# Performance work log

Measured on AMD Instinct MI355X. Metric: run time of the kernel, lower is better.

Reference implementation:

```python
import jax, jax.numpy as jnp
import numpy as np

WS = 2
D = 128  # hidden_dim per direction
SCALE_X = float(np.sqrt(2.0))  # rescale=True, highway_bias=0 -> sqrt(1+exp(0))


def sru_bidir(x, W, wc, b, k):
    """Bidirectional single-layer SRU (sru lib, layer_norm=False, rescale=True).
    x: (L, N, din). Returns (L, N, 2*D)."""
    L, N, _ = x.shape
    U = (x @ W).reshape(L, N, 2, D, k)  # (L,N,dir,D,k)
    vf, vr = wc.reshape(2, 2, D)  # each (dir, D)
    bf, br = b.reshape(2, 2, D)
    # time-reverse the backward direction so one scan handles both
    U = jnp.concatenate([U[:, :, :1], U[::-1, :, 1:]], axis=2)
    if k == 4:
        xprime = U[..., 3]
    else:
        xp = x.reshape(L, N, 2, D)
        xprime = jnp.concatenate([xp[:, :, :1], xp[::-1, :, 1:]], axis=2) * SCALE_X

    def step(c, inp):
        u0, u1, u2, xpt = inp  # each (N,2,D)
        f = jax.nn.sigmoid(u1 + vf * c + bf)
        c = f * c + (1.0 - f) * u0
        r = jax.nn.sigmoid(u2 + vr * c + br)
        h = r * c + (1.0 - r) * xpt
        return c, h

    c0 = jnp.zeros((N, 2, D), dtype=x.dtype)
    _, H = jax.lax.scan(step, c0, (U[..., 0], U[..., 1], U[..., 2], xprime))
    # un-reverse backward direction outputs
    H = jnp.concatenate([H[:, :, :1], H[::-1, :, 1:]], axis=2)
    return H.reshape(L, N, 2 * D)


def setup_inputs() -> dict:
    key = jax.random.key(0)
    ks = jax.random.split(key, 6)
    B, C, Himg, Wimg = 8, 3, 224, 224
    F = WS * WS * C  # 12
    inp = {
        "x": jax.random.normal(ks[0], (B, C, Himg, Wimg), jnp.float32),
        "W1": jax.random.normal(ks[1], (F, 2 * D * 4), jnp.float32) * (1.0 / np.sqrt(F)),
        "wc1": jax.random.normal(ks[2], (2 * 2 * D,), jnp.float32) * 0.1,
        "b1": jnp.zeros((2 * 2 * D,), jnp.float32),
        "W2": jax.random.normal(ks[3], (2 * D, 2 * D * 3), jnp.float32) * (1.0 / np.sqrt(2 * D)),
        "wc2": jax.random.normal(ks[4], (2 * 2 * D,), jnp.float32) * 0.1,
        "b2": jnp.zeros((2 * 2 * D,), jnp.float32),
    }
    return inp


def reference(x, W1, wc1, b1, W2, wc2, b2):
    B, C, Himg, Wimg = x.shape
    Hp, Wp = Himg // WS, Wimg // WS
    F = WS * WS * C
    # get_valid_patches: (B, Hp, Wp, C*ws*ws) with (C, wh, ww) flatten order
    p = x.reshape(B, C, Hp, WS, Wp, WS).transpose(0, 2, 4, 1, 3, 5).reshape(B, Hp, Wp, F)
    # input_array = patches.permute(2,0,3,1) -> (Hp, B, Wp, F)
    # apply_one_direction on firstVRNN: merge Hp into batch, scan over Wp
    a1 = p.transpose(1, 0, 2, 3).reshape(Hp * B, Wp, F).transpose(1, 0, 2)  # (Wp, Hp*B, F)
    h1 = sru_bidir(a1, W1, wc1, b1, k=4)  # (Wp, Hp*B, 2D)
    h1 = h1.transpose(1, 0, 2).reshape(Hp, B, Wp, 2 * D)
    # vertical_results = out.permute(2,1,0,3) -> (Wp, B, Hp, 2D)
    v = h1.transpose(2, 1, 0, 3)
    # second direction: merge Wp into batch, scan over Hp
    a2 = v.reshape(Wp * B, Hp, 2 * D).transpose(1, 0, 2)  # (Hp, Wp*B, 2D)
    h2 = sru_bidir(a2, W2, wc2, b2, k=3)  # (Hp, Wp*B, 2D)
    h2 = h2.transpose(1, 0, 2).reshape(Wp, B, Hp, 2 * D)
    # feature_map.permute(1,3,2,0) -> (B, 2D, Hp, Wp)
    return h2.transpose(1, 3, 2, 0)
```

## Files before the change

### kernel.cpp

```cpp
#include <hip/hip_runtime.h>
#include <hip/hip_bf16.h>

typedef unsigned short ushort_t;
typedef unsigned int uint_t;

typedef __bf16 bf16x8 __attribute__((ext_vector_type(8)));
typedef float f32x4 __attribute__((ext_vector_type(4)));
typedef ushort_t us8 __attribute__((ext_vector_type(8)));

__device__ __forceinline__ float bf2f(ushort_t u) {
    return __uint_as_float(((uint_t)u) << 16);
}
__device__ __forceinline__ ushort_t f2bf(float f) {
    uint_t x = __float_as_uint(f);
    uint_t r = (x + 0x7FFFu + ((x >> 16) & 1u)) >> 16;
    return (ushort_t)r;
}
__device__ __forceinline__ float sigmoidf_fast(float x) {
    return 1.0f / (1.0f + __expf(-x));
}

#define PP 12544
#define PLANE 25690112ULL

__global__ __launch_bounds__(256) void permute_w2(const float* __restrict__ W2,
                                                  ushort_t* __restrict__ W2t) {
    int i = blockIdx.x * 256 + threadIdx.x;
    int np = i >> 8;
    int k  = i & 255;
    int kk  = np >> 8;
    int rem = np & 255;
    int dir = rem >> 7;
    int d   = rem & 127;
    int oc = dir * 384 + d * 3 + kk;
    W2t[np * 256 + k] = f2bf(W2[k * 768 + oc]);
}

__global__ __launch_bounds__(256) void scan1(const float* __restrict__ x,
                                             const float* __restrict__ W1,
                                             const float* __restrict__ wc1,
                                             const float* __restrict__ b1,
                                             ushort_t* __restrict__ H1a) {
    __shared__ float patch[112 * 12];
    const int n1 = blockIdx.x;
    const int hp = n1 >> 3, b = n1 & 7;
    const int tid = threadIdx.x;

    for (int e = tid; e < 1344; e += 256) {
        int c = e / 448;
        int rem = e % 448;
        int wh = rem / 224;
        int pos = rem % 224;
        float v = x[((b * 3 + c) * 224 + (2 * hp + wh)) * 224 + pos];
        patch[(pos >> 1) * 12 + c * 4 + wh * 2 + (pos & 1)] = v;
    }

    float4 w[12];
    const float4* W1v = (const float4*)W1;
#pragma unroll
    for (int j = 0; j < 12; ++j) w[j] = W1v[j * 256 + tid];

    const float vf = wc1[tid],       vr = wc1[256 + tid];
    const float bfv = b1[tid],       brv = b1[256 + tid];
    const int dir = tid >> 7;

    __syncthreads();

    const size_t h1base = ((size_t)b * PP + (size_t)hp * 112) * 256 + tid;

    float cst = 0.0f;
    for (int t = 0; t < 112; ++t) {
        const int tt = dir ? (111 - t) : t;
        const float4* pp = (const float4*)(patch + tt * 12);
        float4 p0 = pp[0], p1 = pp[1], p2 = pp[2];
        float pj[12] = {p0.x, p0.y, p0.z, p0.w, p1.x, p1.y, p1.z, p1.w,
                        p2.x, p2.y, p2.z, p2.w};
        float u0 = 0.f, u1 = 0.f, u2 = 0.f, u3 = 0.f;
#pragma unroll
        for (int j = 0; j < 12; ++j) {
            float pv = pj[j];
            u0 = fmaf(w[j].x, pv, u0);
            u1 = fmaf(w[j].y, pv, u1);
            u2 = fmaf(w[j].z, pv, u2);
            u3 = fmaf(w[j].w, pv, u3);
        }
        float f = sigmoidf_fast(u1 + vf * cst + bfv);
        cst = f * cst + (1.0f - f) * u0;
        float r = sigmoidf_fast(u2 + vr * cst + brv);
        float h = r * cst + (1.0f - r) * u3;
        H1a[h1base + (size_t)tt * 256] = f2bf(h);
    }
}

__global__ __launch_bounds__(256) void gemm2(const ushort_t* __restrict__ A,
                                             const ushort_t* __restrict__ Bt,
                                             ushort_t* __restrict__ U2t) {
    __shared__ ushort_t As[2][128 * 32];
    __shared__ ushort_t Bs[2][128 * 32];

    const int l    = blockIdx.x;
    const int pair = (l & 7) * 588 + (l >> 3);
    const int nx   = pair % 6;
    const int ny   = pair / 6;

    const int m0 = ny * 128;
    const int bb = ny / 98;
    const int p0 = (ny % 98) * 128;
    const int n0 = nx * 128;
    const int kidx = n0 >> 8;
    const int ch0  = n0 & 255;
    const int tid = threadIdx.x;
    const int w = tid >> 6, lane = tid & 63;
    const int wm = w >> 1, wn = w & 1;
    const int lr = lane >> 2;
    const int lc = (lane & 3) * 8;
    const int ln16 = lane & 15;
    const int k8 = (lane >> 4) * 8;

    f32x4 acc[4][4] = {};

    for (int kb = 0; kb < 256; kb += 64) {
        if (kb) __syncthreads();
#pragma unroll
        for (int h = 0; h < 2; ++h) {
#pragma unroll
            for (int q = 0; q < 2; ++q) {
                int r = w * 32 + q * 16;
                const ushort_t* gA = A + (size_t)(m0 + r + lr) * 256 + kb + h * 32 + lc;
                __builtin_amdgcn_global_load_lds(
                    (const __attribute__((address_space(1))) uint_t*)gA,
                    (__attribute__((address_space(3))) uint_t*)(As[h] + r * 32), 16, 0, 0);
                const ushort_t* gB = Bt + (size_t)(n0 + r + lr) * 256 + kb + h * 32 + lc;
                __builtin_amdgcn_global_load_lds(
                    (const __attribute__((address_space(1))) uint_t*)gB,
                    (__attribute__((address_space(3))) uint_t*)(Bs[h] + r * 32), 16, 0, 0);
            }
        }
        __syncthreads();

#pragma unroll
        for (int h = 0; h < 2; ++h) {
            bf16x8 af[4], bf[4];
#pragma unroll
            for (int i = 0; i < 4; ++i) {
                af[i] = *(const bf16x8*)(As[h] + (wm * 64 + i * 16 + ln16) * 32 + k8);
                bf[i] = *(const bf16x8*)(Bs[h] + (wn * 64 + i * 16 + ln16) * 32 + k8);
            }
#pragma unroll
            for (int i = 0; i < 4; ++i)
#pragma unroll
                for (int j = 0; j < 4; ++j)
                    acc[i][j] = __builtin_amdgcn_mfma_f32_16x16x32_bf16(
                        af[i], bf[j], acc[i][j], 0, 0, 0);
        }

        if (nx < 4 && kb == nx * 64) {
            const int cl = tid & 63;
            const int pc = tid >> 6;
            const int hh = cl >> 5;
            const int cc = cl & 31;
            const size_t p3 = 3 * PLANE
                            + (size_t)(bb * 256 + kb + cl) * PP + p0 + pc * 32;
#pragma unroll
            for (int j8 = 0; j8 < 4; ++j8) {
                us8 v;
#pragma unroll
                for (int j = 0; j < 8; ++j)
                    v[j] = As[hh][(pc * 32 + j8 * 8 + j) * 32 + cc];
                *(us8*)(U2t + p3 + j8 * 8) = v;
            }
        }
    }

    const int rq = (lane >> 4) * 4;
    const size_t planeBase = (size_t)kidx * PLANE + (size_t)(bb * 256 + ch0) * PP;
#pragma unroll
    for (int i = 0; i < 4; ++i) {
        int p = p0 + wm * 64 + i * 16 + rq;
#pragma unroll
        for (int j = 0; j < 4; ++j) {
            int ch_l = wn * 64 + j * 16 + ln16;
            ushort4 v;
            v.x = f2bf(acc[i][j][0]);
            v.y = f2bf(acc[i][j][1]);
            v.z = f2bf(acc[i][j][2]);
            v.w = f2bf(acc[i][j][3]);
            *(ushort4*)(U2t + planeBase + (size_t)ch_l * PP + p) = v;
        }
    }
}

__global__ __launch_bounds__(256) void scan2(const ushort_t* __restrict__ U2t,
                                             const float* __restrict__ wc2,
                                             const float* __restrict__ b2,
                                             float* __restrict__ out) {
    const int cb = blockIdx.x;
    const int b  = blockIdx.y;
    const int tid = threadIdx.x;
    const int ch = cb * 2 + (tid >> 7);
    const int wp = tid & 127;
    if (wp >= 112) return;
    const int dir = ch >> 7;
    const float SCALE_X = 1.41421356237309515f;

    const float vf = wc2[ch],  vr = wc2[256 + ch];
    const float bfv = b2[ch],  brv = b2[256 + ch];

    const int tt0 = dir ? 111 : 0;
    const long dstep = dir ? -112 : 112;
    const long ostep = dir ? -112 : 112;

    const ushort_t* P = U2t;
    long oOff = (long)((size_t)(b * 256 + ch) * 112 + tt0) * 112 + wp;

    ushort_t buf[7][4];
    long qp = (long)((size_t)(b * 256 + ch) * PP) + tt0 * 112 + wp;
#pragma unroll
    for (int i = 0; i < 6; ++i) {
        buf[i][0] = P[qp];
        buf[i][1] = P[PLANE + qp];
        buf[i][2] = P[2 * PLANE + qp];
        buf[i][3] = P[3 * PLANE + qp];
        qp += dstep;
    }

    float cst = 0.0f;
    for (int tb = 0; tb < 16; ++tb) {
#pragma unroll
        for (int u = 0; u < 7; ++u) {
            const int t = tb * 7 + u;
            buf[(u + 6) % 7][0] = P[qp];
            buf[(u + 6) % 7][1] = P[PLANE + qp];
            buf[(u + 6) % 7][2] = P[2 * PLANE + qp];
            buf[(u + 6) % 7][3] = P[3 * PLANE + qp];
            qp += (t < 105) ? dstep : 0;

            float u0 = bf2f(buf[u][0]);
            float u1 = bf2f(buf[u][1]);
            float u2v = bf2f(buf[u][2]);
            float xp = bf2f(buf[u][3]) * SCALE_X;
            float f = sigmoidf_fast(u1 + vf * cst + bfv);
            cst = f * cst + (1.0f - f) * u0;
            float r = sigmoidf_fast(u2v + vr * cst + brv);
            out[oOff] = r * cst + (1.0f - r) * xp;
            oOff += ostep;
        }
    }
}

extern "C" void kernel_launch(void* const* d_in, const int* in_sizes, int n_in,
                              void* d_out, int out_size, void* d_ws, size_t ws_size,
                              hipStream_t stream) {
    const float* x   = (const float*)d_in[0];
    const float* W1  = (const float*)d_in[1];
    const float* wc1 = (const float*)d_in[2];
    const float* b1  = (const float*)d_in[3];
    const float* W2  = (const float*)d_in[4];
    const float* wc2 = (const float*)d_in[5];
    const float* b2  = (const float*)d_in[6];
    float* out = (float*)d_out;

    char* ws = (char*)d_ws;
    ushort_t* H1a = (ushort_t*)(ws);
    ushort_t* U2t = (ushort_t*)(ws + 51380224);
    ushort_t* W2t = (ushort_t*)(ws + 51380224 + 205520896);

    permute_w2<<<768, 256, 0, stream>>>(W2, W2t);
    scan1<<<896, 256, 0, stream>>>(x, W1, wc1, b1, H1a);
    gemm2<<<4704, 256, 0, stream>>>(H1a, W2t, U2t);
    scan2<<<dim3(128, 8), 256, 0, stream>>>(U2t, wc2, b2, out);
}
```

Measured before the change: 353.2 us.

## Double-buffer GEMM K-loop with 32-wide stages to overlap loads and MFMA

Restructures the second-layer GEMM main loop from four 64-wide K blocks, each fully loaded before compute, into eight 32-wide stages with ping-pong LDS buffers. The next stage's global-to-LDS loads are issued before the current stage's MFMAs, so memory latency can hide behind compute. Global pointers are hoisted out of the loop, and the x-prime copy-out is adapted to 32-column stages. The cost is more barriers per tile and shallower compute per stage.

```diff
diff --git a/kernel.cpp b/kernel.cpp
--- a/kernel.cpp
+++ b/kernel.cpp
@@ -117,60 +117,76 @@
     const int ln16 = lane & 15;
     const int k8 = (lane >> 4) * 8;
 
+    const int r0 = w * 32;
+    const ushort_t* gA0 = A  + (size_t)(m0 + r0 + lr) * 256 + lc;
+    const ushort_t* gA1 = A  + (size_t)(m0 + r0 + 16 + lr) * 256 + lc;
+    const ushort_t* gB0 = Bt + (size_t)(n0 + r0 + lr) * 256 + lc;
+    const ushort_t* gB1 = Bt + (size_t)(n0 + r0 + 16 + lr) * 256 + lc;
+
     f32x4 acc[4][4] = {};
 
-    for (int kb = 0; kb < 256; kb += 64) {
-        if (kb) __syncthreads();
-#pragma unroll
-        for (int h = 0; h < 2; ++h) {
-#pragma unroll
-            for (int q = 0; q < 2; ++q) {
-                int r = w * 32 + q * 16;
-                const ushort_t* gA = A + (size_t)(m0 + r + lr) * 256 + kb + h * 32 + lc;
-                __builtin_amdgcn_global_load_lds(
-                    (const __attribute__((address_space(1))) uint_t*)gA,
-                    (__attribute__((address_space(3))) uint_t*)(As[h] + r * 32), 16, 0, 0);
-                const ushort_t* gB = Bt + (size_t)(n0 + r + lr) * 256 + kb + h * 32 + lc;
-                __builtin_amdgcn_global_load_lds(
-                    (const __attribute__((address_space(1))) uint_t*)gB,
-                    (__attribute__((address_space(3))) uint_t*)(Bs[h] + r * 32), 16, 0, 0);
-            }
-        }
-        __syncthreads();
-
-#pragma unroll
-        for (int h = 0; h < 2; ++h) {
-            bf16x8 af[4], bf[4];
-#pragma unroll
-            for (int i = 0; i < 4; ++i) {
-                af[i] = *(const bf16x8*)(As[h] + (wm * 64 + i * 16 + ln16) * 32 + k8);
-                bf[i] = *(const bf16x8*)(Bs[h] + (wn * 64 + i * 16 + ln16) * 32 + k8);
-            }
-#pragma unroll
-            for (int i = 0; i < 4; ++i)
-#pragma unroll
-                for (int j = 0; j < 4; ++j)
-                    acc[i][j] = __builtin_amdgcn_mfma_f32_16x16x32_bf16(
-                        af[i], bf[j], acc[i][j], 0, 0, 0);
-        }
-
-        if (nx < 4 && kb == nx * 64) {
-            const int cl = tid & 63;
-            const int pc = tid >> 6;
-            const int hh = cl >> 5;
-            const int cc = cl & 31;
+#define STAGE(bufi, s32)                                                      \
+    do {                                                                      \
+        const int kc_ = (s32) * 32;                                           \
+        __builtin_amdgcn_global_load_lds(                                     \
+            (const __attribute__((address_space(1))) uint_t*)(gA0 + kc_),     \
+            (__attribute__((address_space(3))) uint_t*)(As[bufi] + r0 * 32),  \
+            16, 0, 0);                                                        \
+        __builtin_amdgcn_global_load_lds(                                     \
+            (const __attribute__((address_space(1))) uint_t*)(gA1 + kc_),     \
+            (__attribute__((address_space(3))) uint_t*)(As[bufi] + (r0 + 16) * 32), \
+            16, 0, 0);                                                        \
+        __builtin_amdgcn_global_load_lds(                                     \
+            (const __attribute__((address_space(1))) uint_t*)(gB0 + kc_),     \
+            (__attribute__((address_space(3))) uint_t*)(Bs[bufi] + r0 * 32),  \
+            16, 0, 0);                                                        \
+        __builtin_amdgcn_global_load_lds(                                     \
+            (const __attribute__((address_space(1))) uint_t*)(gB1 + kc_),     \
+            (__attribute__((address_space(3))) uint_t*)(Bs[bufi] + (r0 + 16) * 32), \
+            16, 0, 0);                                                        \
+    } while (0)
+
+    STAGE(0, 0);
+    asm volatile("s_waitcnt vmcnt(0)" ::: "memory");
+    __builtin_amdgcn_s_barrier();
+
+    for (int s = 0; s < 8; ++s) {
+        const int cur = s & 1;
+        if (s < 7) STAGE(cur ^ 1, s + 1);
+
+        bf16x8 af[4], bfr[4];
+#pragma unroll
+        for (int i = 0; i < 4; ++i) {
+            af[i]  = *(const bf16x8*)(As[cur] + (wm * 64 + i * 16 + ln16) * 32 + k8);
+            bfr[i] = *(const bf16x8*)(Bs[cur] + (wn * 64 + i * 16 + ln16) * 32 + k8);
+        }
+#pragma unroll
+        for (int i = 0; i < 4; ++i)
+#pragma unroll
+            for (int j = 0; j < 4; ++j)
+                acc[i][j] = __builtin_amdgcn_mfma_f32_16x16x32_bf16(
+                    af[i], bfr[j], acc[i][j], 0, 0, 0);
+
+        if (nx < 4 && (s >> 1) == nx) {
+            const int cl = tid & 31;
+            const int pc = tid >> 5;
             const size_t p3 = 3 * PLANE
-                            + (size_t)(bb * 256 + kb + cl) * PP + p0 + pc * 32;
-#pragma unroll
-            for (int j8 = 0; j8 < 4; ++j8) {
+                            + (size_t)(bb * 256 + s * 32 + cl) * PP
+                            + p0 + pc * 16;
+#pragma unroll
+            for (int j8 = 0; j8 < 2; ++j8) {
                 us8 v;
 #pragma unroll
                 for (int j = 0; j < 8; ++j)
-                    v[j] = As[hh][(pc * 32 + j8 * 8 + j) * 32 + cc];
+                    v[j] = As[cur][(pc * 16 + j8 * 8 + j) * 32 + cl];
                 *(us8*)(U2t + p3 + j8 * 8) = v;
             }
         }
-    }
+
+        asm volatile("s_waitcnt vmcnt(0)" ::: "memory");
+        __builtin_amdgcn_s_barrier();
+    }
+#undef STAGE
 
     const int rq = (lane >> 4) * 4;
     const size_t planeBase = (size_t)kidx * PLANE + (size_t)(bb * 256 + ch0) * PP;
```

New measurement: 364.2 us. 1.03x slower.
